# Kernel tuning notes

Measured on AMD Instinct MI355X. Metric: run time of the kernel, lower is better.

The kernel has to match this reference:

```python
import jax, jax.numpy as jnp
import numpy as np

DIM = 2048
N_HEADS = 16
KV_HEADS = 2 * 2  # 4
HEAD_DIM = DIM // N_HEADS  # 128
B, T = 2, 2048


def apply_rope(x, cos, sin):
    # Faithful to the source: x is replaced by its rotated version, then
    # multiplied by (sin + cos). x: [B,H,T,D], cos/sin: [T,D] broadcast.
    x1 = x[..., ::2]
    x2 = x[..., 1::2]
    rot = jnp.stack((-x2, x1), axis=-1).reshape(x.shape)
    return rot * sin + rot * cos


def setup_inputs() -> dict:
    key = jax.random.key(0)
    ks = jax.random.split(key, 8)
    x = jax.random.normal(ks[0], (B, T, DIM), dtype=jnp.float32)
    cos = jax.random.uniform(ks[1], (T, HEAD_DIM), dtype=jnp.float32)
    sin = jax.random.uniform(ks[2], (T, HEAD_DIM), dtype=jnp.float32)
    mask = jnp.tril(jnp.ones((T, T), dtype=bool))  # causal
    s = 1.0 / np.sqrt(DIM)
    Wq = jax.random.normal(ks[3], (DIM, DIM), dtype=jnp.float32) * s
    Wk = jax.random.normal(ks[4], (KV_HEADS * HEAD_DIM, DIM), dtype=jnp.float32) * s
    Wv = jax.random.normal(ks[5], (KV_HEADS * HEAD_DIM, DIM), dtype=jnp.float32) * s
    Wout = jax.random.normal(ks[6], (DIM, DIM), dtype=jnp.float32) * s
    bout = jax.random.normal(ks[7], (DIM,), dtype=jnp.float32) * s
    return {"x": x, "cos": cos, "sin": sin, "mask": mask,
            "Wq": Wq, "Wk": Wk, "Wv": Wv, "Wout": Wout, "bout": bout}


def reference(x, cos, sin, mask, Wq, Wk, Wv, Wout, bout):
    Bb, Tt, C = x.shape
    # projections (torch Linear: x @ W.T)
    q = (x @ Wq.T).reshape(Bb, Tt, N_HEADS, HEAD_DIM).transpose(0, 2, 1, 3)
    k = (x @ Wk.T).reshape(Bb, Tt, KV_HEADS, HEAD_DIM).transpose(0, 2, 1, 3)
    v = (x @ Wv.T).reshape(Bb, Tt, KV_HEADS, HEAD_DIM).transpose(0, 2, 1, 3)
    q = apply_rope(q, cos, sin)
    k = apply_rope(k, cos, sin)
    repeat = N_HEADS // KV_HEADS
    k = jnp.repeat(k, repeat, axis=1)  # [B,H,T,D]
    v = jnp.repeat(v, repeat, axis=1)
    attn = jnp.einsum("bhtd,bhsd->bhts", q, k) / np.sqrt(HEAD_DIM)
    attn = jnp.where(mask, attn, jnp.float32(-1e9))
    probs = jax.nn.softmax(attn, axis=-1)
    out = jnp.einsum("bhts,bhsd->bhtd", probs, v)
    out = out.transpose(0, 2, 1, 3).reshape(Bb, Tt, C)
    return out @ Wout.T + bout
```

## Files before the change

kernel.cpp:

```cpp
#include <hip/hip_runtime.h>
#include <type_traits>

#define DEVI __device__ __forceinline__

typedef unsigned short u16;
typedef unsigned int u32;
typedef float f32x4 __attribute__((ext_vector_type(4)));
typedef __bf16 bf16x8 __attribute__((ext_vector_type(8)));
typedef unsigned short u16x4 __attribute__((ext_vector_type(4)));
typedef unsigned short u16x8 __attribute__((ext_vector_type(8)));
typedef unsigned int u32x2 __attribute__((ext_vector_type(2)));

constexpr int BATCH = 2;
constexpr int T     = 2048;
constexpr int DIM   = 2048;
constexpr int NH    = 16;
constexpr int KVH   = 4;
constexpr int HD    = 128;
constexpr int NQKV  = DIM + 2 * KVH * HD;
constexpr int ROWS  = BATCH * T;
constexpr float SC2 = 0.08838834764831845f * 1.4426950408889634f;

DEVI u16 f2b(float f) {
  u32 u = __float_as_uint(f);
  return (u16)((u + 0x7fffu + ((u >> 16) & 1u)) >> 16);
}
DEVI float b2f(u16 u) { return __uint_as_float(((u32)u) << 16); }

DEVI u32 cvtpk(float lo, float hi) {
  u32 r;
  asm("v_cvt_pk_bf16_f32 %0, %1, %2" : "=v"(r) : "v"(lo), "v"(hi));
  return r;
}

DEVI f32x4 mfma16(bf16x8 a, bf16x8 b, f32x4 c) {
  return __builtin_amdgcn_mfma_f32_16x16x32_bf16(a, b, c, 0, 0, 0);
}
DEVI void gload16(const void* g, void* l) {
  __builtin_amdgcn_global_load_lds((const __attribute__((address_space(1))) void*)g,
                                   (__attribute__((address_space(3))) void*)l, 16, 0, 0);
}

__global__ void cvt_all_kernel(const float* __restrict__ x,
                               const float* __restrict__ Wq, const float* __restrict__ Wk,
                               const float* __restrict__ Wv, const float* __restrict__ Wo,
                               const float* __restrict__ cosp, const float* __restrict__ sinp,
                               u16* __restrict__ xb, u16* __restrict__ wqkv,
                               u16* __restrict__ wout, float* __restrict__ cs)
{
  constexpr int S0 = ROWS * DIM / 4;
  constexpr int S1 = DIM * DIM / 4;
  constexpr int S2 = 512 * DIM / 4;
  constexpr int S3 = 512 * DIM / 4;
  constexpr int S4 = DIM * DIM / 4;
  constexpr int S5 = T * HD / 4;
  int i = blockIdx.x * 256 + threadIdx.x;
  const float* src; u16* dst;
  if (i < S0) { src = x; dst = xb; }
  else if ((i -= S0) < S1) { src = Wq; dst = wqkv; }
  else if ((i -= S1) < S2) { src = Wk; dst = wqkv + DIM * DIM; }
  else if ((i -= S2) < S3) { src = Wv; dst = wqkv + (size_t)(DIM + 512) * DIM; }
  else if ((i -= S3) < S4) { src = Wo; dst = wout; }
  else if ((i -= S4) < S5) {
    float4 c = ((const float4*)cosp)[i];
    float4 s = ((const float4*)sinp)[i];
    float4 o = { c.x + s.x, c.y + s.y, c.z + s.z, c.w + s.w };
    ((float4*)cs)[i] = o;
    return;
  } else return;
  float4 v = ((const float4*)src)[i];
  u16x4 o = { f2b(v.x), f2b(v.y), f2b(v.z), f2b(v.w) };
  ((u16x4*)dst)[i] = o;
}

template<bool BF16OUT, bool BIAS>
__global__ __launch_bounds__(256) void gemm_bt_kernel(
    const u16* __restrict__ A, const u16* __restrict__ W,
    void* __restrict__ Cout, const float* __restrict__ bias,
    int M, int N, int K)
{
  constexpr int BK = 64;
  __shared__ u16 sA[128 * BK];
  __shared__ u16 sB[128 * BK];
  const int nbx = N >> 7;
  const int bx = blockIdx.x % nbx;
  const int by = blockIdx.x / nbx;
  const int m0 = by << 7, n0 = bx << 7;
  const int tid = threadIdx.x;
  const int w = tid >> 6, lane = tid & 63;
  const int wr = w >> 1, wc = w & 1;
  const int lq = lane & 15, lg = lane >> 4;

  f32x4 acc[4][4] = {};

  int srow[4], scb[4];
#pragma unroll
  for (int c = 0; c < 4; ++c) {
    int off = (w * 4 + c) * 1024 + lane * 16;
    srow[c] = off >> 7;
    scb[c]  = (off & 127) ^ ((srow[c] & 7) << 4);
  }

  for (int kt = 0; kt < K; kt += BK) {
#pragma unroll
    for (int c = 0; c < 4; ++c) {
      u16* la = sA + (w * 4 + c) * 512;
      u16* lb = sB + (w * 4 + c) * 512;
      gload16(A + (size_t)(m0 + srow[c]) * K + kt + (scb[c] >> 1), la);
      gload16(W + (size_t)(n0 + srow[c]) * K + kt + (scb[c] >> 1), lb);
    }
    __syncthreads();
#pragma unroll
    for (int ks = 0; ks < 2; ++ks) {
      bf16x8 af[4], bfr[4];
#pragma unroll
      for (int i = 0; i < 4; ++i) {
        int ra = wr * 64 + i * 16 + lq;
        int ca = (ks * 64 + lg * 16) ^ ((ra & 7) << 4);
        af[i] = *(const bf16x8*)((const char*)sA + ra * 128 + ca);
        int rb = wc * 64 + i * 16 + lq;
        int cb = (ks * 64 + lg * 16) ^ ((rb & 7) << 4);
        bfr[i] = *(const bf16x8*)((const char*)sB + rb * 128 + cb);
      }
#pragma unroll
      for (int i = 0; i < 4; ++i)
#pragma unroll
        for (int j = 0; j < 4; ++j)
          acc[i][j] = mfma16(af[i], bfr[j], acc[i][j]);
    }
    __syncthreads();
  }

  const int crow = m0 + wr * 64 + lg * 4;
  const int ccol = n0 + wc * 64 + lq;
#pragma unroll
  for (int j = 0; j < 4; ++j) {
    int col = ccol + j * 16;
    float bv = BIAS ? bias[col] : 0.0f;
#pragma unroll
    for (int i = 0; i < 4; ++i)
#pragma unroll
      for (int r = 0; r < 4; ++r) {
        size_t idx = (size_t)(crow + i * 16 + r) * N + col;
        float v = acc[i][j][r] + bv;
        if (BF16OUT) ((u16*)Cout)[idx] = f2b(v);
        else         ((float*)Cout)[idx] = v;
      }
  }
}

__global__ void rope_k_kernel(const u16* __restrict__ Y, const float* __restrict__ cs,
                              u16* __restrict__ kr)
{
  int pid = blockIdx.x * 256 + threadIdx.x;
  int i  = pid & 63;
  int hr = pid >> 6;
  int h  = hr & (KVH - 1);
  int r  = hr / KVH;
  int t  = r & (T - 1);
  int b  = r >> 11;
  u32 y = *(const u32*)(Y + (size_t)r * NQKV + DIM + h * HD + 2 * i);
  float y0 = b2f((u16)(y & 0xffffu));
  float y1 = b2f((u16)(y >> 16));
  const float* cp = cs + t * HD + 2 * i;
  u32 o = (u32)f2b(-y1 * cp[0]) | ((u32)f2b(y0 * cp[1]) << 16);
  *(u32*)(kr + (((size_t)(b * KVH + h) * T + t) * HD + 2 * i)) = o;
}

__global__ __launch_bounds__(256) void vt_kernel(const u16* __restrict__ Y, u16* __restrict__ vt)
{
  __shared__ u16 tile[64][136];
  const int tid = threadIdx.x;
  const int tc = blockIdx.x & 31;
  const int kh = (blockIdx.x >> 5) & 3;
  const int b  = blockIdx.x >> 7;
  const u16* src = Y + (size_t)(b * T + tc * 64) * NQKV + (DIM + KVH * HD) + kh * HD;
#pragma unroll
  for (int pass = 0; pass < 4; ++pass) {
    int r = pass * 16 + (tid >> 4);
    int c = (tid & 15) * 8;
    *(u16x8*)&tile[r][c] = *(const u16x8*)(src + (size_t)r * NQKV + c);
  }
  __syncthreads();
  const int d = tid >> 1, th = tid & 1;
  u16* dst = vt + ((size_t)((b * KVH + kh) * HD + d) * T) + tc * 64 + th * 32;
#pragma unroll
  for (int j = 0; j < 4; ++j) {
    u16x8 v;
#pragma unroll
    for (int e = 0; e < 8; ++e) v[e] = tile[th * 32 + j * 8 + e][d];
    *(u16x8*)(dst + j * 8) = v;
  }
}

__global__ __launch_bounds__(256, 2) void attn_kernel(
    const u16* __restrict__ Y, const float* __restrict__ cs,
    const u16* __restrict__ Kr, const u16* __restrict__ Vt,
    u16* __restrict__ Aout)
{
  __shared__ u16 ldsK[64 * 128];
  __shared__ u16 ldsV[128 * 64];
  __shared__ u16 ldsP[4][32 * 40];

  const int tid = threadIdx.x;
  const int w = tid >> 6, lane = tid & 63;
  const int lq = lane & 15, lg = lane >> 4;

  const int s  = blockIdx.x & 255;
  const int r0 = blockIdx.x >> 8;
  const int x  = s & 7;
  const int j  = s >> 3;
  const int bh = (x >> 2) * 16 + (x & 3) * 4 + (j & 3);
  const int p  = r0 ? (8 + (j >> 2)) : (j >> 2);
  const int b = bh >> 4, h = bh & 15, kh = h >> 2;
  const int qcA = p, qcB = 31 - p;
  const int rowA = qcA * 64 + w * 16;
  const int rowB = qcB * 64 + w * 16;
  const int nst = qcB + 1;

  bf16x8 qf[2][4];
#pragma unroll
  for (int qg = 0; qg < 2; ++qg) {
    const int rowX = qg ? rowB : rowA;
    const u16* yp = Y + ((size_t)(b * T + rowX + lq)) * NQKV + h * HD + lg * 8;
    const float* cp = cs + (rowX + lq) * HD + lg * 8;
#pragma unroll
    for (int ds = 0; ds < 4; ++ds) {
      u16x8 y = *(const u16x8*)(yp + ds * 32);
      float4 c0 = *(const float4*)(cp + ds * 32);
      float4 c1 = *(const float4*)(cp + ds * 32 + 4);
      u16x8 o;
      o[0] = f2b(-b2f(y[1]) * c0.x * SC2); o[1] = f2b(b2f(y[0]) * c0.y * SC2);
      o[2] = f2b(-b2f(y[3]) * c0.z * SC2); o[3] = f2b(b2f(y[2]) * c0.w * SC2);
      o[4] = f2b(-b2f(y[5]) * c1.x * SC2); o[5] = f2b(b2f(y[4]) * c1.y * SC2);
      o[6] = f2b(-b2f(y[7]) * c1.z * SC2); o[7] = f2b(b2f(y[6]) * c1.w * SC2);
      qf[qg][ds] = *(bf16x8*)&o;
    }
  }

  const u16* Kg = Kr + (size_t)(b * KVH + kh) * T * HD;
  const u16* Vg = Vt + (size_t)(b * KVH + kh) * HD * T;

  int kgo[4], klb[4], vgo[4], vlb[4];
  {
    const int vr = lane >> 3, vc = lane & 7;
#pragma unroll
    for (int i = 0; i < 4; ++i) {
      int krow = w * 16 + i * 4 + lg;
      kgo[i] = krow * HD + (((lq * 16) ^ ((krow & 7) << 4)) >> 1);
      klb[i] = (w * 16 + i * 4) * 128;
      int vrow = w * 32 + i * 8 + vr;
      vgo[i] = vrow * T + (((vc * 16) ^ ((vr & 7) << 4)) >> 1);
      vlb[i] = (w * 32 + i * 8) * 64;
    }
  }

  f32x4 accO[2][8] = {};
  float lsum[2] = { 0.f, 0.f };

#pragma unroll
  for (int i = 0; i < 4; ++i) gload16(Kg + kgo[i], &ldsK[klb[i]]);
  __syncthreads();

  for (int t = 0; t < nst; ++t) {
    const int s0 = t << 6;

    {
      const u16* Vts = Vg + t * 64;
#pragma unroll
      for (int i = 0; i < 4; ++i) gload16(Vts + vgo[i], &ldsV[vlb[i]]);
    }

    auto softmax_qg = [&](f32x4 (&s4)[4], int qidx, bool diag, float& ls,
                          float (&pp)[16]) {
      if (diag) {
#pragma unroll
        for (int si = 0; si < 4; ++si)
#pragma unroll
          for (int r = 0; r < 4; ++r) {
            int sidx = s0 + si * 16 + lg * 4 + r;
            pp[si * 4 + r] = (sidx <= qidx) ? __builtin_amdgcn_exp2f(s4[si][r]) : 0.0f;
          }
      } else {
#pragma unroll
        for (int si = 0; si < 4; ++si)
#pragma unroll
          for (int r = 0; r < 4; ++r)
            pp[si * 4 + r] = __builtin_amdgcn_exp2f(s4[si][r]);
      }
      float ps = 0.f;
#pragma unroll
      for (int i2 = 0; i2 < 16; ++i2) ps += pp[i2];
      ls += ps;
    };

    float pp[2][16];
    const bool hasA = (t <= qcA);

    auto qk_phase = [&](auto hasA_c) {
      constexpr bool HASA = decltype(hasA_c)::value;
      f32x4 aS[2][4] = {};
#pragma unroll
      for (int si = 0; si < 4; ++si)
#pragma unroll
        for (int ds = 0; ds < 4; ++ds) {
          const u16* kp = ldsK + (si * 16 + lq) * 128 +
                          (((ds * 64 + lg * 16) ^ ((lq & 7) << 4)) >> 1);
          bf16x8 kf = *(const bf16x8*)kp;
          if constexpr (HASA) aS[0][si] = mfma16(kf, qf[0][ds], aS[0][si]);
          aS[1][si] = mfma16(kf, qf[1][ds], aS[1][si]);
        }
      if constexpr (HASA)
        softmax_qg(aS[0], rowA + lq, t == qcA, lsum[0], pp[0]);
      softmax_qg(aS[1], rowB + lq, t == qcB, lsum[1], pp[1]);
    };
    if (hasA) qk_phase(std::integral_constant<bool, true>{});
    else      qk_phase(std::integral_constant<bool, false>{});

    __syncthreads();

    if (t + 1 < nst) {
      const u16* Kt = Kg + (size_t)(t + 1) * 64 * HD;
#pragma unroll
      for (int i = 0; i < 4; ++i) gload16(Kt + kgo[i], &ldsK[klb[i]]);
    }

    auto pv_phase = [&](auto hasA_c) {
      constexpr bool HASA = decltype(hasA_c)::value;
#pragma unroll
      for (int ks = 0; ks < 2; ++ks) {
        if constexpr (HASA) {
          u16* pw = &ldsP[w][lq * 40];
          u32x2 wa = { cvtpk(pp[0][8 * ks + 0], pp[0][8 * ks + 1]),
                       cvtpk(pp[0][8 * ks + 2], pp[0][8 * ks + 3]) };
          u32x2 wb = { cvtpk(pp[0][8 * ks + 4], pp[0][8 * ks + 5]),
                       cvtpk(pp[0][8 * ks + 6], pp[0][8 * ks + 7]) };
          *(u32x2*)(pw + lg * 4)      = wa;
          *(u32x2*)(pw + 16 + lg * 4) = wb;
        }
        {
          u16* pw = &ldsP[w][(16 + lq) * 40];
          u32x2 wa = { cvtpk(pp[1][8 * ks + 0], pp[1][8 * ks + 1]),
                       cvtpk(pp[1][8 * ks + 2], pp[1][8 * ks + 3]) };
          u32x2 wb = { cvtpk(pp[1][8 * ks + 4], pp[1][8 * ks + 5]),
                       cvtpk(pp[1][8 * ks + 6], pp[1][8 * ks + 7]) };
          *(u32x2*)(pw + lg * 4)      = wa;
          *(u32x2*)(pw + 16 + lg * 4) = wb;
        }
        asm volatile("" ::: "memory");
        bf16x8 pf0, pf1;
        if constexpr (HASA) pf0 = *(const bf16x8*)(&ldsP[w][lq * 40] + lg * 8);
        pf1 = *(const bf16x8*)(&ldsP[w][(16 + lq) * 40] + lg * 8);
        asm volatile("" ::: "memory");
#pragma unroll
        for (int db = 0; db < 8; ++db) {
          const u16* vp = ldsV + (db * 16 + lq) * 64 +
                          (((ks * 64 + lg * 16) ^ ((lq & 7) << 4)) >> 1);
          bf16x8 vf = *(const bf16x8*)vp;
          if constexpr (HASA) accO[0][db] = mfma16(vf, pf0, accO[0][db]);
          accO[1][db] = mfma16(vf, pf1, accO[1][db]);
        }
      }
    };
    if (hasA) pv_phase(std::integral_constant<bool, true>{});
    else      pv_phase(std::integral_constant<bool, false>{});

    __syncthreads();
  }

#pragma unroll
  for (int qg = 0; qg < 2; ++qg) {
    const int rowX = qg ? rowB : rowA;
    float l = qg ? lsum[1] : lsum[0];
    l += __shfl_xor(l, 16);
    l += __shfl_xor(l, 32);
    float inv = 1.0f / l;
    u16* Ab = Aout + ((size_t)b * T + rowX + lq) * DIM + h * HD;
#pragma unroll
    for (int db = 0; db < 8; ++db) {
      f32x4 a = qg ? accO[1][db] : accO[0][db];
      u32x2 st = { cvtpk(a[0] * inv, a[1] * inv),
                   cvtpk(a[2] * inv, a[3] * inv) };
      *(u32x2*)(Ab + db * 16 + lg * 4) = st;
    }
  }
}

extern "C" void kernel_launch(void* const* d_in, const int* in_sizes, int n_in,
                              void* d_out, int out_size, void* d_ws, size_t ws_size,
                              hipStream_t stream) {
  const float* x    = (const float*)d_in[0];
  const float* cosp = (const float*)d_in[1];
  const float* sinp = (const float*)d_in[2];
  const float* Wq   = (const float*)d_in[4];
  const float* Wk   = (const float*)d_in[5];
  const float* Wv   = (const float*)d_in[6];
  const float* Wo   = (const float*)d_in[7];
  const float* bo   = (const float*)d_in[8];

  char* ws = (char*)d_ws;
  u16*   xb   = (u16*)(ws + 0);
  u16*   wqkv = (u16*)(ws + 16777216);
  u16*   wout = (u16*)(ws + 29360128);
  float* cs   = (float*)(ws + 37748736);
  u16*   yqkv = (u16*)(ws + 38797312);
  u16*   kr   = (u16*)(ws + 63963136);
  u16*   vt   = (u16*)(ws + 68157440);
  u16* aout = xb;

  constexpr int CVT_TOTAL = ROWS * DIM / 4 + DIM * DIM / 4 + 512 * DIM / 4 * 2
                          + DIM * DIM / 4 + T * HD / 4;
  cvt_all_kernel<<<(CVT_TOTAL + 255) / 256, 256, 0, stream>>>(
      x, Wq, Wk, Wv, Wo, cosp, sinp, xb, wqkv, wout, cs);

  gemm_bt_kernel<true, false><<<(ROWS / 128) * (NQKV / 128), 256, 0, stream>>>(
      xb, wqkv, yqkv, nullptr, ROWS, NQKV, DIM);

  rope_k_kernel<<<ROWS * KVH * 64 / 256, 256, 0, stream>>>(yqkv, cs, kr);
  vt_kernel<<<BATCH * KVH * (T / 64), 256, 0, stream>>>(yqkv, vt);

  attn_kernel<<<BATCH * NH * 16, 256, 0, stream>>>(yqkv, cs, kr, vt, aout);

  gemm_bt_kernel<false, true><<<(ROWS / 128) * (DIM / 128), 256, 0, stream>>>(
      aout, wout, d_out, bo, ROWS, DIM, DIM);
}
```

Measured before the change: 192.2 us.

## Split paired q-chunk attention blocks into one q-chunk per block

Each attention block previously handled two query chunks paired for causal load balance (p and 31-p), sharing K/V tiles across both. Now each block handles one 64-row query chunk, the grid doubles to 1024 blocks, and launch bounds go from 2 to 4 blocks per CU to allow more occupancy with fewer registers. This gives up K/V LDS reuse across the two chunks and the built-in load balance, relying on the scheduler to take longest chunks first (qc = 31 - j/4), in exchange for more parallelism and lower per-block register pressure.

```diff
diff --git a/kernel.cpp b/kernel.cpp
--- a/kernel.cpp
+++ b/kernel.cpp
@@ -193,37 +193,31 @@
   }
 }
 
-__global__ __launch_bounds__(256, 2) void attn_kernel(
+__global__ __launch_bounds__(256, 4) void attn_kernel(
     const u16* __restrict__ Y, const float* __restrict__ cs,
     const u16* __restrict__ Kr, const u16* __restrict__ Vt,
     u16* __restrict__ Aout)
 {
   __shared__ u16 ldsK[64 * 128];
   __shared__ u16 ldsV[128 * 64];
-  __shared__ u16 ldsP[4][32 * 40];
+  __shared__ u16 ldsP[4][16 * 40];
 
   const int tid = threadIdx.x;
   const int w = tid >> 6, lane = tid & 63;
   const int lq = lane & 15, lg = lane >> 4;
 
-  const int s  = blockIdx.x & 255;
-  const int r0 = blockIdx.x >> 8;
-  const int x  = s & 7;
-  const int j  = s >> 3;
+  const int x  = blockIdx.x & 7;
+  const int j  = blockIdx.x >> 3;
   const int bh = (x >> 2) * 16 + (x & 3) * 4 + (j & 3);
-  const int p  = r0 ? (8 + (j >> 2)) : (j >> 2);
+  const int qc = 31 - (j >> 2);
   const int b = bh >> 4, h = bh & 15, kh = h >> 2;
-  const int qcA = p, qcB = 31 - p;
-  const int rowA = qcA * 64 + w * 16;
-  const int rowB = qcB * 64 + w * 16;
-  const int nst = qcB + 1;
-
-  bf16x8 qf[2][4];
-#pragma unroll
-  for (int qg = 0; qg < 2; ++qg) {
-    const int rowX = qg ? rowB : rowA;
-    const u16* yp = Y + ((size_t)(b * T + rowX + lq)) * NQKV + h * HD + lg * 8;
-    const float* cp = cs + (rowX + lq) * HD + lg * 8;
+  const int rowQ = qc * 64 + w * 16;
+  const int nst = qc + 1;
+
+  bf16x8 qf[4];
+  {
+    const u16* yp = Y + ((size_t)(b * T + rowQ + lq)) * NQKV + h * HD + lg * 8;
+    const float* cp = cs + (rowQ + lq) * HD + lg * 8;
 #pragma unroll
     for (int ds = 0; ds < 4; ++ds) {
       u16x8 y = *(const u16x8*)(yp + ds * 32);
@@ -234,7 +228,7 @@
       o[2] = f2b(-b2f(y[3]) * c0.z * SC2); o[3] = f2b(b2f(y[2]) * c0.w * SC2);
       o[4] = f2b(-b2f(y[5]) * c1.x * SC2); o[5] = f2b(b2f(y[4]) * c1.y * SC2);
       o[6] = f2b(-b2f(y[7]) * c1.z * SC2); o[7] = f2b(b2f(y[6]) * c1.w * SC2);
-      qf[qg][ds] = *(bf16x8*)&o;
+      qf[ds] = *(bf16x8*)&o;
     }
   }
 
@@ -255,8 +249,8 @@
     }
   }
 
-  f32x4 accO[2][8] = {};
-  float lsum[2] = { 0.f, 0.f };
+  f32x4 accO[8] = {};
+  float lsum = 0.f;
 
 #pragma unroll
   for (int i = 0; i < 4; ++i) gload16(Kg + kgo[i], &ldsK[klb[i]]);
@@ -271,35 +265,9 @@
       for (int i = 0; i < 4; ++i) gload16(Vts + vgo[i], &ldsV[vlb[i]]);
     }
 
-    auto softmax_qg = [&](f32x4 (&s4)[4], int qidx, bool diag, float& ls,
-                          float (&pp)[16]) {
-      if (diag) {
-#pragma unroll
-        for (int si = 0; si < 4; ++si)
-#pragma unroll
-          for (int r = 0; r < 4; ++r) {
-            int sidx = s0 + si * 16 + lg * 4 + r;
-            pp[si * 4 + r] = (sidx <= qidx) ? __builtin_amdgcn_exp2f(s4[si][r]) : 0.0f;
-          }
-      } else {
-#pragma unroll
-        for (int si = 0; si < 4; ++si)
-#pragma unroll
-          for (int r = 0; r < 4; ++r)
-            pp[si * 4 + r] = __builtin_amdgcn_exp2f(s4[si][r]);
-      }
-      float ps = 0.f;
-#pragma unroll
-      for (int i2 = 0; i2 < 16; ++i2) ps += pp[i2];
-      ls += ps;
-    };
-
-    float pp[2][16];
-    const bool hasA = (t <= qcA);
-
-    auto qk_phase = [&](auto hasA_c) {
-      constexpr bool HASA = decltype(hasA_c)::value;
-      f32x4 aS[2][4] = {};
+    float pp[16];
+    {
+      f32x4 aS[4] = {};
 #pragma unroll
       for (int si = 0; si < 4; ++si)
 #pragma unroll
@@ -307,15 +275,29 @@
           const u16* kp = ldsK + (si * 16 + lq) * 128 +
                           (((ds * 64 + lg * 16) ^ ((lq & 7) << 4)) >> 1);
           bf16x8 kf = *(const bf16x8*)kp;
-          if constexpr (HASA) aS[0][si] = mfma16(kf, qf[0][ds], aS[0][si]);
-          aS[1][si] = mfma16(kf, qf[1][ds], aS[1][si]);
+          aS[si] = mfma16(kf, qf[ds], aS[si]);
         }
-      if constexpr (HASA)
-        softmax_qg(aS[0], rowA + lq, t == qcA, lsum[0], pp[0]);
-      softmax_qg(aS[1], rowB + lq, t == qcB, lsum[1], pp[1]);
-    };
-    if (hasA) qk_phase(std::integral_constant<bool, true>{});
-    else      qk_phase(std::integral_constant<bool, false>{});
+      const int qidx = rowQ + lq;
+      if (t == qc) {
+#pragma unroll
+        for (int si = 0; si < 4; ++si)
+#pragma unroll
+          for (int r = 0; r < 4; ++r) {
+            int sidx = s0 + si * 16 + lg * 4 + r;
+            pp[si * 4 + r] = (sidx <= qidx) ? __builtin_amdgcn_exp2f(aS[si][r]) : 0.0f;
+          }
+      } else {
+#pragma unroll
+        for (int si = 0; si < 4; ++si)
+#pragma unroll
+          for (int r = 0; r < 4; ++r)
+            pp[si * 4 + r] = __builtin_amdgcn_exp2f(aS[si][r]);
+      }
+      float ps = 0.f;
+#pragma unroll
+      for (int i2 = 0; i2 < 16; ++i2) ps += pp[i2];
+      lsum += ps;
+    }
 
     __syncthreads();
 
@@ -325,62 +307,42 @@
       for (int i = 0; i < 4; ++i) gload16(Kt + kgo[i], &ldsK[klb[i]]);
     }
 
-    auto pv_phase = [&](auto hasA_c) {
-      constexpr bool HASA = decltype(hasA_c)::value;
-#pragma unroll
-      for (int ks = 0; ks < 2; ++ks) {
-        if constexpr (HASA) {
-          u16* pw = &ldsP[w][lq * 40];
-          u32x2 wa = { cvtpk(pp[0][8 * ks + 0], pp[0][8 * ks + 1]),
-                       cvtpk(pp[0][8 * ks + 2], pp[0][8 * ks + 3]) };
-          u32x2 wb = { cvtpk(pp[0][8 * ks + 4], pp[0][8 * ks + 5]),
-                       cvtpk(pp[0][8 * ks + 6], pp[0][8 * ks + 7]) };
-          *(u32x2*)(pw + lg * 4)      = wa;
-          *(u32x2*)(pw + 16 + lg * 4) = wb;
-        }
-        {
-          u16* pw = &ldsP[w][(16 + lq) * 40];
-          u32x2 wa = { cvtpk(pp[1][8 * ks + 0], pp[1][8 * ks + 1]),
-                       cvtpk(pp[1][8 * ks + 2], pp[1][8 * ks + 3]) };
-          u32x2 wb = { cvtpk(pp[1][8 * ks + 4], pp[1][8 * ks + 5]),
-                       cvtpk(pp[1][8 * ks + 6], pp[1][8 * ks + 7]) };
-          *(u32x2*)(pw + lg * 4)      = wa;
-          *(u32x2*)(pw + 16 + lg * 4) = wb;
-        }
-        asm volatile("" ::: "memory");
-        bf16x8 pf0, pf1;
-        if constexpr (HASA) pf0 = *(const bf16x8*)(&ldsP[w][lq * 40] + lg * 8);
-        pf1 = *(const bf16x8*)(&ldsP[w][(16 + lq) * 40] + lg * 8);
-        asm volatile("" ::: "memory");
-#pragma unroll
-        for (int db = 0; db < 8; ++db) {
-          const u16* vp = ldsV + (db * 16 + lq) * 64 +
-                          (((ks * 64 + lg * 16) ^ ((lq & 7) << 4)) >> 1);
-          bf16x8 vf = *(const bf16x8*)vp;
-          if constexpr (HASA) accO[0][db] = mfma16(vf, pf0, accO[0][db]);
-          accO[1][db] = mfma16(vf, pf1, accO[1][db]);
-        }
-      }
-    };
-    if (hasA) pv_phase(std::integral_constant<bool, true>{});
-    else      pv_phase(std::integral_constant<bool, false>{});
+#pragma unroll
+    for (int ks = 0; ks < 2; ++ks) {
+      {
+        u16* pw = &ldsP[w][lq * 40];
+        u32x2 wa = { cvtpk(pp[8 * ks + 0], pp[8 * ks + 1]),
+                     cvtpk(pp[8 * ks + 2], pp[8 * ks + 3]) };
+        u32x2 wb = { cvtpk(pp[8 * ks + 4], pp[8 * ks + 5]),
+                     cvtpk(pp[8 * ks + 6], pp[8 * ks + 7]) };
+        *(u32x2*)(pw + lg * 4)      = wa;
+        *(u32x2*)(pw + 16 + lg * 4) = wb;
+      }
+      asm volatile("" ::: "memory");
+      bf16x8 pf = *(const bf16x8*)(&ldsP[w][lq * 40] + lg * 8);
+      asm volatile("" ::: "memory");
+#pragma unroll
+      for (int db = 0; db < 8; ++db) {
+        const u16* vp = ldsV + (db * 16 + lq) * 64 +
+                        (((ks * 64 + lg * 16) ^ ((lq & 7) << 4)) >> 1);
+        bf16x8 vf = *(const bf16x8*)vp;
+        accO[db] = mfma16(vf, pf, accO[db]);
+      }
+    }
 
     __syncthreads();
   }
 
-#pragma unroll
-  for (int qg = 0; qg < 2; ++qg) {
-    const int rowX = qg ? rowB : rowA;
-    float l = qg ? lsum[1] : lsum[0];
+  {
+    float l = lsum;
     l += __shfl_xor(l, 16);
     l += __shfl_xor(l, 32);
     float inv = 1.0f / l;
-    u16* Ab = Aout + ((size_t)b * T + rowX + lq) * DIM + h * HD;
+    u16* Ab = Aout + ((size_t)b * T + rowQ + lq) * DIM + h * HD;
 #pragma unroll
     for (int db = 0; db < 8; ++db) {
-      f32x4 a = qg ? accO[1][db] : accO[0][db];
-      u32x2 st = { cvtpk(a[0] * inv, a[1] * inv),
-                   cvtpk(a[2] * inv, a[3] * inv) };
+      u32x2 st = { cvtpk(accO[db][0] * inv, accO[db][1] * inv),
+                   cvtpk(accO[db][2] * inv, accO[db][3] * inv) };
       *(u32x2*)(Ab + db * 16 + lg * 4) = st;
     }
   }
@@ -419,7 +381,7 @@
   rope_k_kernel<<<ROWS * KVH * 64 / 256, 256, 0, stream>>>(yqkv, cs, kr);
   vt_kernel<<<BATCH * KVH * (T / 64), 256, 0, stream>>>(yqkv, vt);
 
-  attn_kernel<<<BATCH * NH * 16, 256, 0, stream>>>(yqkv, cs, kr, vt, aout);
+  attn_kernel<<<BATCH * NH * 32, 256, 0, stream>>>(yqkv, cs, kr, vt, aout);
 
   gemm_bt_kernel<false, true><<<(ROWS / 128) * (DIM / 128), 256, 0, stream>>>(
       aout, wout, d_out, bo, ROWS, DIM, DIM);
```

Result: no change. 194.9 us (+1.4%).

## Double attention KV tile to 128 keys, pack probabilities early, add setprio

Applied to the files above, without the earlier changes.

Raises the key/value tile processed per loop iteration from 64 to 128 keys. This halves the number of barrier-separated iterations and the per-iteration load/sync overhead, while doubling the K and V LDS buffers to 64 KB total. Softmax probabilities are now converted to packed bf16 right after the exponent instead of inside the PV phase. The MFMA sections are also wrapped in s_setprio so waves issuing matrix ops get scheduling priority. The costs are coarser causal granularity, so the diagonal tile does more masked wasted work, and higher LDS and register pressure that may reduce occupancy below 2 blocks per CU.

```diff
diff --git a/kernel.cpp b/kernel.cpp
--- a/kernel.cpp
+++ b/kernel.cpp
@@ -198,8 +198,8 @@
     const u16* __restrict__ Kr, const u16* __restrict__ Vt,
     u16* __restrict__ Aout)
 {
-  __shared__ u16 ldsK[64 * 128];
-  __shared__ u16 ldsV[128 * 64];
+  __shared__ u16 ldsK[128 * 128];
+  __shared__ u16 ldsV[128 * 128];
   __shared__ u16 ldsP[4][32 * 40];
 
   const int tid = threadIdx.x;
@@ -216,7 +216,9 @@
   const int qcA = p, qcB = 31 - p;
   const int rowA = qcA * 64 + w * 16;
   const int rowB = qcB * 64 + w * 16;
-  const int nst = qcB + 1;
+  const int tA = (qcA * 64 + 63) >> 7;
+  const int tB = (qcB * 64 + 63) >> 7;
+  const int nst = tB + 1;
 
   bf16x8 qf[2][4];
 #pragma unroll
@@ -241,67 +243,43 @@
   const u16* Kg = Kr + (size_t)(b * KVH + kh) * T * HD;
   const u16* Vg = Vt + (size_t)(b * KVH + kh) * HD * T;
 
-  int kgo[4], klb[4], vgo[4], vlb[4];
-  {
-    const int vr = lane >> 3, vc = lane & 7;
-#pragma unroll
-    for (int i = 0; i < 4; ++i) {
-      int krow = w * 16 + i * 4 + lg;
-      kgo[i] = krow * HD + (((lq * 16) ^ ((krow & 7) << 4)) >> 1);
-      klb[i] = (w * 16 + i * 4) * 128;
-      int vrow = w * 32 + i * 8 + vr;
-      vgo[i] = vrow * T + (((vc * 16) ^ ((vr & 7) << 4)) >> 1);
-      vlb[i] = (w * 32 + i * 8) * 64;
-    }
+  int kgo[8], klb[8], vgo[8];
+#pragma unroll
+  for (int i = 0; i < 8; ++i) {
+    int row = w * 32 + i * 4 + lg;
+    int scol = ((lq * 16) ^ ((row & 7) << 4)) >> 1;
+    kgo[i] = row * HD + scol;
+    vgo[i] = row * T + scol;
+    klb[i] = (w * 32 + i * 4) * 128;
   }
 
   f32x4 accO[2][8] = {};
   float lsum[2] = { 0.f, 0.f };
 
 #pragma unroll
-  for (int i = 0; i < 4; ++i) gload16(Kg + kgo[i], &ldsK[klb[i]]);
+  for (int i = 0; i < 8; ++i) gload16(Kg + kgo[i], &ldsK[klb[i]]);
   __syncthreads();
 
   for (int t = 0; t < nst; ++t) {
-    const int s0 = t << 6;
+    const int s0 = t << 7;
 
     {
-      const u16* Vts = Vg + t * 64;
-#pragma unroll
-      for (int i = 0; i < 4; ++i) gload16(Vts + vgo[i], &ldsV[vlb[i]]);
-    }
-
-    auto softmax_qg = [&](f32x4 (&s4)[4], int qidx, bool diag, float& ls,
-                          float (&pp)[16]) {
-      if (diag) {
-#pragma unroll
-        for (int si = 0; si < 4; ++si)
-#pragma unroll
-          for (int r = 0; r < 4; ++r) {
-            int sidx = s0 + si * 16 + lg * 4 + r;
-            pp[si * 4 + r] = (sidx <= qidx) ? __builtin_amdgcn_exp2f(s4[si][r]) : 0.0f;
-          }
-      } else {
-#pragma unroll
-        for (int si = 0; si < 4; ++si)
-#pragma unroll
-          for (int r = 0; r < 4; ++r)
-            pp[si * 4 + r] = __builtin_amdgcn_exp2f(s4[si][r]);
-      }
-      float ps = 0.f;
-#pragma unroll
-      for (int i2 = 0; i2 < 16; ++i2) ps += pp[i2];
-      ls += ps;
-    };
-
-    float pp[2][16];
-    const bool hasA = (t <= qcA);
+      const u16* Vts = Vg + s0;
+#pragma unroll
+      for (int i = 0; i < 8; ++i) gload16(Vts + vgo[i], &ldsV[klb[i]]);
+    }
+
+    u32 pkw[2][8][2];
+    const bool hasA = (t <= tA);
 
     auto qk_phase = [&](auto hasA_c) {
       constexpr bool HASA = decltype(hasA_c)::value;
-      f32x4 aS[2][4] = {};
-#pragma unroll
-      for (int si = 0; si < 4; ++si)
+      f32x4 aS[2][8];
+#pragma unroll
+      for (int si = 0; si < 8; ++si) { aS[0][si] = f32x4{0,0,0,0}; aS[1][si] = f32x4{0,0,0,0}; }
+      __builtin_amdgcn_s_setprio(1);
+#pragma unroll
+      for (int si = 0; si < 8; ++si)
 #pragma unroll
         for (int ds = 0; ds < 4; ++ds) {
           const u16* kp = ldsK + (si * 16 + lq) * 128 +
@@ -310,9 +288,33 @@
           if constexpr (HASA) aS[0][si] = mfma16(kf, qf[0][ds], aS[0][si]);
           aS[1][si] = mfma16(kf, qf[1][ds], aS[1][si]);
         }
-      if constexpr (HASA)
-        softmax_qg(aS[0], rowA + lq, t == qcA, lsum[0], pp[0]);
-      softmax_qg(aS[1], rowB + lq, t == qcB, lsum[1], pp[1]);
+      __builtin_amdgcn_s_setprio(0);
+
+#pragma unroll
+      for (int qg = 0; qg < 2; ++qg) {
+        if (!HASA && qg == 0) continue;
+        const int qidx = (qg ? rowB : rowA) + lq;
+        const bool diag = (t == (qg ? tB : tA));
+        float ps = 0.f;
+#pragma unroll
+        for (int si = 0; si < 8; ++si) {
+          float e[4];
+#pragma unroll
+          for (int r = 0; r < 4; ++r) {
+            float v = aS[qg][si][r];
+            if (diag) {
+              int sidx = s0 + si * 16 + lg * 4 + r;
+              e[r] = (sidx <= qidx) ? __builtin_amdgcn_exp2f(v) : 0.0f;
+            } else {
+              e[r] = __builtin_amdgcn_exp2f(v);
+            }
+            ps += e[r];
+          }
+          pkw[qg][si][0] = cvtpk(e[0], e[1]);
+          pkw[qg][si][1] = cvtpk(e[2], e[3]);
+        }
+        lsum[qg] += ps;
+      }
     };
     if (hasA) qk_phase(std::integral_constant<bool, true>{});
     else      qk_phase(std::integral_constant<bool, false>{});
@@ -320,30 +322,26 @@
     __syncthreads();
 
     if (t + 1 < nst) {
-      const u16* Kt = Kg + (size_t)(t + 1) * 64 * HD;
-#pragma unroll
-      for (int i = 0; i < 4; ++i) gload16(Kt + kgo[i], &ldsK[klb[i]]);
+      const u16* Kt = Kg + (size_t)(t + 1) * 128 * HD;
+#pragma unroll
+      for (int i = 0; i < 8; ++i) gload16(Kt + kgo[i], &ldsK[klb[i]]);
     }
 
     auto pv_phase = [&](auto hasA_c) {
       constexpr bool HASA = decltype(hasA_c)::value;
 #pragma unroll
-      for (int ks = 0; ks < 2; ++ks) {
+      for (int hh = 0; hh < 4; ++hh) {
         if constexpr (HASA) {
           u16* pw = &ldsP[w][lq * 40];
-          u32x2 wa = { cvtpk(pp[0][8 * ks + 0], pp[0][8 * ks + 1]),
-                       cvtpk(pp[0][8 * ks + 2], pp[0][8 * ks + 3]) };
-          u32x2 wb = { cvtpk(pp[0][8 * ks + 4], pp[0][8 * ks + 5]),
-                       cvtpk(pp[0][8 * ks + 6], pp[0][8 * ks + 7]) };
+          u32x2 wa = { pkw[0][2 * hh][0],     pkw[0][2 * hh][1] };
+          u32x2 wb = { pkw[0][2 * hh + 1][0], pkw[0][2 * hh + 1][1] };
           *(u32x2*)(pw + lg * 4)      = wa;
           *(u32x2*)(pw + 16 + lg * 4) = wb;
         }
         {
           u16* pw = &ldsP[w][(16 + lq) * 40];
-          u32x2 wa = { cvtpk(pp[1][8 * ks + 0], pp[1][8 * ks + 1]),
-                       cvtpk(pp[1][8 * ks + 2], pp[1][8 * ks + 3]) };
-          u32x2 wb = { cvtpk(pp[1][8 * ks + 4], pp[1][8 * ks + 5]),
-                       cvtpk(pp[1][8 * ks + 6], pp[1][8 * ks + 7]) };
+          u32x2 wa = { pkw[1][2 * hh][0],     pkw[1][2 * hh][1] };
+          u32x2 wb = { pkw[1][2 * hh + 1][0], pkw[1][2 * hh + 1][1] };
           *(u32x2*)(pw + lg * 4)      = wa;
           *(u32x2*)(pw + 16 + lg * 4) = wb;
         }
@@ -352,14 +350,16 @@
         if constexpr (HASA) pf0 = *(const bf16x8*)(&ldsP[w][lq * 40] + lg * 8);
         pf1 = *(const bf16x8*)(&ldsP[w][(16 + lq) * 40] + lg * 8);
         asm volatile("" ::: "memory");
+        __builtin_amdgcn_s_setprio(1);
 #pragma unroll
         for (int db = 0; db < 8; ++db) {
-          const u16* vp = ldsV + (db * 16 + lq) * 64 +
-                          (((ks * 64 + lg * 16) ^ ((lq & 7) << 4)) >> 1);
+          const u16* vp = ldsV + (db * 16 + lq) * 128 +
+                          (((hh * 64 + lg * 16) ^ ((lq & 7) << 4)) >> 1);
           bf16x8 vf = *(const bf16x8*)vp;
           if constexpr (HASA) accO[0][db] = mfma16(vf, pf0, accO[0][db]);
           accO[1][db] = mfma16(vf, pf1, accO[1][db]);
         }
+        __builtin_amdgcn_s_setprio(0);
       }
     };
     if (hasA) pv_phase(std::integral_constant<bool, true>{});
```

Measured after the change: 255.5 us. 32.9% more time.
